# Kernel optimization log

Measured on AMD Instinct MI355X. Metric: run time of the kernel, lower is better.

Reference implementation:

```python
import jax, jax.numpy as jnp
import numpy as np

HIDDEN = 4096
N_HEADS = 32
N_KV_HEADS = 8
HEAD_DIM = 128
ROPE_THETA = 10000.0
LCK = 3          # number of suffix KV blocks
B = 2
S = 1024         # Q_LEN
VALID = 960      # valid_seq_len
NEG = -1e30


def rotate_half(x):
    h = x.shape[-1] // 2
    return jnp.concatenate([-x[..., h:], x[..., :h]], axis=-1)


def rope_cos_sin(seq_len, dim, theta, dtype):
    inv_freq = 1.0 / (theta ** (jnp.arange(0, dim, 2, dtype=jnp.float32) / dim))
    pos = jnp.arange(seq_len, dtype=jnp.float32)
    freqs = pos[:, None] * inv_freq[None, :]          # [S, dim/2]
    emb = jnp.concatenate([freqs, freqs], axis=-1)    # [S, dim]
    return jnp.cos(emb).astype(dtype), jnp.sin(emb).astype(dtype)


def setup_inputs() -> dict:
    key = jax.random.key(0)
    ks = jax.random.split(key, 8)
    w = 0.02
    return {
        "hidden_states": jax.random.normal(ks[0], (B, S, HIDDEN), jnp.float32),
        "k_suffix": jax.random.normal(ks[1], (B, N_KV_HEADS, LCK, S, HEAD_DIM), jnp.float32),
        "v_suffix": jax.random.normal(ks[2], (B, N_KV_HEADS, LCK, S, HEAD_DIM), jnp.float32),
        "Wq": jax.random.normal(ks[3], (HIDDEN, N_HEADS * HEAD_DIM), jnp.float32) * w,
        "Wk": jax.random.normal(ks[4], (HIDDEN, N_KV_HEADS * HEAD_DIM), jnp.float32) * w,
        "Wv": jax.random.normal(ks[5], (HIDDEN, N_KV_HEADS * HEAD_DIM), jnp.float32) * w,
        "Wo": jax.random.normal(ks[6], (N_HEADS * HEAD_DIM, HIDDEN), jnp.float32) * w,
        "valid_seq_len": VALID,
    }


def reference(hidden_states, k_suffix, v_suffix, Wq, Wk, Wv, Wo, valid_seq_len):
    b, s, _ = hidden_states.shape
    lck = k_suffix.shape[2]
    n_rep = N_HEADS // N_KV_HEADS
    scale = 1.0 / np.sqrt(HEAD_DIM)

    # projections: [B, H, S, D]
    q = (hidden_states @ Wq).reshape(b, s, N_HEADS, HEAD_DIM).transpose(0, 2, 1, 3)
    k0 = (hidden_states @ Wk).reshape(b, s, N_KV_HEADS, HEAD_DIM).transpose(0, 2, 1, 3)
    v0 = (hidden_states @ Wv).reshape(b, s, N_KV_HEADS, HEAD_DIM).transpose(0, 2, 1, 3)

    # RoPE on fresh q / k0
    cos, sin = rope_cos_sin(s, HEAD_DIM, ROPE_THETA, q.dtype)
    cos = cos[None, None]
    sin = sin[None, None]
    q = q * cos + rotate_half(q) * sin
    k0 = k0 * cos + rotate_half(k0) * sin

    # GQA expansion (repeat_kv)
    k0r = jnp.repeat(k0, n_rep, axis=1)                 # [B, H, S, D]
    v0r = jnp.repeat(v0, n_rep, axis=1)
    ks = jnp.repeat(k_suffix, n_rep, axis=1)            # [B, H, lck, S, D]
    vs = jnp.repeat(v_suffix, n_rep, axis=1)

    q_idx = jnp.arange(s)
    q_valid = q_idx < valid_seq_len                     # [S]

    # --- causal block (kv_idx < Q_LEN) ---
    sc_c = jnp.einsum('bhqd,bhkd->bhqk', q, k0r) * scale
    mask_c = (q_idx[:, None] >= q_idx[None, :]) & q_valid[None, :] & q_valid[:, None]
    sc_c = jnp.where(mask_c[None, None], sc_c, NEG)

    # --- suffix blocks: only diagonal kv_idx = q_idx + j*Q_LEN survives ---
    # score for suffix block j at query q is q . k_suffix[j, q]
    sc_s = jnp.einsum('bhqd,bhjqd->bhqj', q, ks) * scale    # [B, H, S, lck]
    # diag kv_mod == q_idx, so suffix valid iff q_idx < valid_seq_len
    sc_s = jnp.where(q_valid[None, None, :, None], sc_s, NEG)

    logits = jnp.concatenate([sc_c, sc_s], axis=-1)      # [B, H, S, S+lck]
    probs = jax.nn.softmax(logits, axis=-1)

    out = jnp.einsum('bhqk,bhkd->bhqd', probs[..., :s], v0r) + \
          jnp.einsum('bhqj,bhjqd->bhqd', probs[..., s:], vs)
    # fully-masked rows (q >= valid_seq_len) output zero like flash attention
    out = out * q_valid[None, None, :, None].astype(out.dtype)

    out = out.transpose(0, 2, 1, 3).reshape(b, s, N_HEADS * HEAD_DIM)
    return out @ Wo


if __name__ == "__main__":
    o = reference(**setup_inputs())
    print(o.shape, o.dtype)
```

## Files before the change

### kernel.cpp

```cpp
#include <hip/hip_runtime.h>

#define HIDDEN 4096
#define NH 32
#define NKV 8
#define HD 128
#define LCK 3
#define BB 2
#define SS 1024
#define MTOT (BB * SS)

typedef unsigned short u16;
typedef __attribute__((ext_vector_type(8))) short s16x8;
typedef __attribute__((ext_vector_type(4))) short s16x4;
typedef __attribute__((ext_vector_type(4))) float f32x4;

__device__ __forceinline__ u16 f2bf(float f) {
  unsigned u = __builtin_bit_cast(unsigned, f);
  u += 0x7fffu + ((u >> 16) & 1u);
  return (u16)(u >> 16);
}
__device__ __forceinline__ float bf2f(u16 h) {
  return __builtin_bit_cast(float, (unsigned)h << 16);
}
__device__ __forceinline__ void gld16(const void* g, void* l) {
  __builtin_amdgcn_global_load_lds((const __attribute__((address_space(1))) void*)g,
                                   (__attribute__((address_space(3))) void*)l, 16, 0, 0);
}

__global__ __launch_bounds__(256) void convert_h(const float* __restrict__ in,
                                                 u16* __restrict__ out, int n4) {
  int i = blockIdx.x * 256 + threadIdx.x;
  if (i >= n4) return;
  float4 v = ((const float4*)in)[i];
  uint2 o;
  o.x = (unsigned)f2bf(v.x) | ((unsigned)f2bf(v.y) << 16);
  o.y = (unsigned)f2bf(v.z) | ((unsigned)f2bf(v.w) << 16);
  ((uint2*)out)[i] = o;
}

__global__ __launch_bounds__(256) void transpose_w(const float* __restrict__ W,
                                                   u16* __restrict__ Wt, int K, int N) {
  __shared__ float tile[64][65];
  const int n0 = blockIdx.x * 64, k0 = blockIdx.y * 64;
  const int ty = threadIdx.x >> 6, tx = threadIdx.x & 63;
#pragma unroll
  for (int i = 0; i < 16; ++i) {
    int r = ty * 16 + i;
    tile[r][tx] = W[(size_t)(k0 + r) * N + n0 + tx];
  }
  __syncthreads();
#pragma unroll
  for (int i = 0; i < 16; ++i) {
    int r = ty * 16 + i;
    Wt[(size_t)(n0 + r) * K + k0 + tx] = f2bf(tile[tx][r]);
  }
}

template <bool BF16OUT>
__global__ __launch_bounds__(512, 2) void gemm_bt(
    const u16* __restrict__ A, const u16* __restrict__ Bt,
    void* C0v, void* C1v, void* C2v, int N, int K, int n1, int n2) {
  __shared__ __align__(16) char smem[131072];
  const int tid = threadIdx.x, lane = tid & 63, w = tid >> 6;
  const int wr = w >> 2, wc = w & 3;
  const int col16 = lane & 15, quad = lane >> 4;

  const int nbx = gridDim.x;
  const int nwg = nbx * gridDim.y;
  int fid = blockIdx.y * nbx + blockIdx.x;
  {
    const int q = nwg >> 3, r = nwg & 7;
    const int xcd = fid & 7, lid = fid >> 3;
    fid = (xcd < r ? xcd * (q + 1) : r * (q + 1) + (xcd - r) * q) + lid;
  }
  const int bm = (fid / nbx) << 8, bn = (fid % nbx) << 8;

  const int rowlane = lane >> 2;
  const int collane = ((lane & 3) * 8) ^ ((lane & 32) ? 16 : 0);
  const u16* aSrc = A + (size_t)(bm + ((w >> 1) << 4) + rowlane) * K + ((w & 1) << 5) + collane;
  const u16* bSrc = Bt + (size_t)(bn + ((w >> 1) << 4) + rowlane) * K + ((w & 1) << 5) + collane;
  const int laneoff = (lane & 15) * 64 + (((lane >> 4) << 4) ^ ((lane & 8) << 2));
  const int NT = K >> 6;

#define STG(opOfs, src, buf, h, tt)                                              \
  do {                                                                           \
    gld16((src) + (size_t)((h) * 128) * K + (size_t)(tt) * 64,                   \
          smem + (buf) * 65536 + (opOfs) +                                       \
              ((((h) * 8 + (w >> 1)) * 2 + (w & 1)) << 10));                     \
    gld16((src) + (size_t)((h) * 128 + 64) * K + (size_t)(tt) * 64,              \
          smem + (buf) * 65536 + (opOfs) +                                       \
              ((((h) * 8 + 4 + (w >> 1)) * 2 + (w & 1)) << 10));                 \
  } while (0)
#define BARX asm volatile("s_barrier" ::: "memory")
#define LGK0                                                                     \
  do {                                                                           \
    asm volatile("s_waitcnt lgkmcnt(0)" ::: "memory");                           \
    __builtin_amdgcn_sched_barrier(0);                                           \
  } while (0)

  f32x4 acc[8][4];
#pragma unroll
  for (int f = 0; f < 8; ++f)
#pragma unroll
    for (int g = 0; g < 4; ++g) acc[f][g] = (f32x4){0.f, 0.f, 0.f, 0.f};

  STG(32768, bSrc, 0, 0, 0);
  STG(32768, bSrc, 0, 1, 0);
  STG(0, aSrc, 0, 0, 0);
  STG(0, aSrc, 0, 1, 0);
  STG(32768, bSrc, 1, 0, 1);
  STG(32768, bSrc, 1, 1, 1);
  STG(0, aSrc, 1, 0, 1);
  asm volatile("s_waitcnt vmcnt(6)" ::: "memory");
  BARX;

  for (int kt = 0; kt < NT; ++kt) {
    const int buf = kt & 1;
    const char* Af = smem + buf * 65536 + wr * 16384 + laneoff;
    const char* Bf = smem + buf * 65536 + 32768 + wc * 8192 + laneoff;
    s16x8 b0[4], b1[4], a0[4], a1[4];
#pragma unroll
    for (int g = 0; g < 4; ++g) {
      b0[g] = *(const s16x8*)(Bf + (g * 2 + 0) * 1024);
      b1[g] = *(const s16x8*)(Bf + (g * 2 + 1) * 1024);
    }
#pragma unroll
    for (int f = 0; f < 4; ++f) a0[f] = *(const s16x8*)(Af + (f * 2 + 0) * 1024);
    if (kt + 1 < NT) STG(0, aSrc, (kt + 1) & 1, 1, kt + 1);
    BARX; LGK0;
    __builtin_amdgcn_s_setprio(1);
#pragma unroll
    for (int f = 0; f < 4; ++f)
#pragma unroll
      for (int g = 0; g < 4; ++g)
        acc[f][g] = __builtin_amdgcn_mfma_f32_16x16x32_bf16(a0[f], b0[g], acc[f][g], 0, 0, 0);
    __builtin_amdgcn_s_setprio(0);
    BARX;
#pragma unroll
    for (int f = 0; f < 4; ++f) a1[f] = *(const s16x8*)(Af + ((4 + f) * 2 + 0) * 1024);
#pragma unroll
    for (int f = 0; f < 4; ++f) a0[f] = *(const s16x8*)(Af + (f * 2 + 1) * 1024);
    if (kt + 2 < NT) STG(32768, bSrc, buf, 0, kt + 2);
    BARX; LGK0;
    __builtin_amdgcn_s_setprio(1);
#pragma unroll
    for (int f = 0; f < 4; ++f)
#pragma unroll
      for (int g = 0; g < 4; ++g)
        acc[4 + f][g] = __builtin_amdgcn_mfma_f32_16x16x32_bf16(a1[f], b0[g], acc[4 + f][g], 0, 0, 0);
    __builtin_amdgcn_s_setprio(0);
    BARX;
#pragma unroll
    for (int f = 0; f < 4; ++f) a1[f] = *(const s16x8*)(Af + ((4 + f) * 2 + 1) * 1024);
    if (kt + 2 < NT) STG(32768, bSrc, buf, 1, kt + 2);
    BARX; LGK0;
    __builtin_amdgcn_s_setprio(1);
#pragma unroll
    for (int f = 0; f < 4; ++f)
#pragma unroll
      for (int g = 0; g < 4; ++g)
        acc[f][g] = __builtin_amdgcn_mfma_f32_16x16x32_bf16(a0[f], b1[g], acc[f][g], 0, 0, 0);
    __builtin_amdgcn_s_setprio(0);
    BARX;
    if (kt + 2 < NT) STG(0, aSrc, buf, 0, kt + 2);
    BARX; LGK0;
    __builtin_amdgcn_s_setprio(1);
#pragma unroll
    for (int f = 0; f < 4; ++f)
#pragma unroll
      for (int g = 0; g < 4; ++g)
        acc[4 + f][g] = __builtin_amdgcn_mfma_f32_16x16x32_bf16(a1[f], b1[g], acc[4 + f][g], 0, 0, 0);
    __builtin_amdgcn_s_setprio(0);
    if (kt < NT - 2) asm volatile("s_waitcnt vmcnt(6)" ::: "memory");
    else if (kt == NT - 2) asm volatile("s_waitcnt vmcnt(0)" ::: "memory");
    BARX;
  }
#undef STG
#undef BARX
#undef LGK0

  float* Cf; u16* Ch; int ldc, nb;
  if (bn < n1)      { ldc = n1;      nb = bn;      Cf = (float*)C0v; Ch = (u16*)C0v; }
  else if (bn < n2) { ldc = n2 - n1; nb = bn - n1; Cf = (float*)C1v; Ch = (u16*)C1v; }
  else              { ldc = N - n2;  nb = bn - n2; Cf = (float*)C2v; Ch = (u16*)C2v; }
#pragma unroll
  for (int f = 0; f < 8; ++f)
#pragma unroll
    for (int g = 0; g < 4; ++g)
#pragma unroll
      for (int r = 0; r < 4; ++r) {
        size_t off = (size_t)(bm + wr * 128 + f * 16 + quad * 4 + r) * ldc +
                     nb + wc * 64 + g * 16 + col16;
        if (BF16OUT) Ch[off] = f2bf(acc[f][g][r]);
        else         Cf[off] = acc[f][g][r];
      }
}

__global__ __launch_bounds__(256) void rope_convert(const u16* __restrict__ Qin,
                                                    const u16* __restrict__ Kin,
                                                    u16* __restrict__ Qout,
                                                    u16* __restrict__ Kout) {
  const int per_row = (NH + NKV) * 64;
  int idx = blockIdx.x * 256 + threadIdx.x;
  if (idx >= MTOT * per_row) return;
  int row = idx / per_row;
  int rem = idx - row * per_row;
  int hh = rem >> 6, i = rem & 63;
  int s = row & (SS - 1), b = row >> 10;

  float invf = __expf((float)i * (-9.210340371976184f / 64.0f));
  float ang = (float)s * invf;
  float cv = cosf(ang), sv = sinf(ang);

  if (hh < NH) {
    const u16* src = Qin + (size_t)row * (NH * HD) + hh * HD;
    u16* dst = Qout + (((size_t)(b * NH + hh)) * SS + s) * HD;
    float x0 = bf2f(src[i]), x1 = bf2f(src[i + 64]);
    dst[i] = f2bf(x0 * cv - x1 * sv);
    dst[i + 64] = f2bf(x1 * cv + x0 * sv);
  } else {
    int kh = hh - NH;
    const u16* src = Kin + (size_t)row * (NKV * HD) + kh * HD;
    u16* dst = Kout + (((size_t)(b * NKV + kh)) * SS + s) * HD;
    float x0 = bf2f(src[i]), x1 = bf2f(src[i + 64]);
    dst[i] = f2bf(x0 * cv - x1 * sv);
    dst[i + 64] = f2bf(x1 * cv + x0 * sv);
  }
}

__global__ __launch_bounds__(256) void transpose_v(const u16* __restrict__ V0,
                                                   u16* __restrict__ Vt) {
  __shared__ u16 tile[64][65];
  const int s0 = blockIdx.x * 64, d0 = blockIdx.y * 64;
  const int bk = blockIdx.z;
  const int b = bk >> 3, kvh = bk & 7;
  const int ty = threadIdx.x >> 6, tx = threadIdx.x & 63;
#pragma unroll
  for (int i = 0; i < 16; ++i) {
    int r = ty * 16 + i;
    tile[r][tx] = V0[((size_t)(b * SS + s0 + r)) * (NKV * HD) + kvh * HD + d0 + tx];
  }
  __syncthreads();
#pragma unroll
  for (int i = 0; i < 16; ++i) {
    int r = ty * 16 + i;
    Vt[((size_t)bk * HD + d0 + r) * SS + s0 + tx] = tile[tx][r];
  }
}

__global__ __launch_bounds__(256) void attn_mfma(
    const u16* __restrict__ Qbf, const u16* __restrict__ Kbf, const u16* __restrict__ Vt,
    const float* __restrict__ ksuf, const float* __restrict__ vsuf,
    u16* __restrict__ AObf, const int* __restrict__ validp) {
  __shared__ __align__(16) char Ksm[2][16384];
  __shared__ __align__(16) char Vsm[2][16384];

  const int bid = (int)blockIdx.x;
  const int qt = 63 - (bid >> 4);
  const int kvh = bid & 7, b = (bid >> 3) & 1;
  const int q0 = qt * 16;
  const int lane = threadIdx.x & 63, w = threadIdx.x >> 6;
  const int col = lane & 15, quad = lane >> 4;
  const int h = (kvh << 2) + w;
  const int valid = *validp;
  const int q = q0 + col;

  size_t orow = ((size_t)(b * SS + q)) * (NH * HD) + h * HD;
  if (q0 >= valid) {
    ushort4 z = {0, 0, 0, 0};
#pragma unroll
    for (int nt = 0; nt < 8; ++nt)
      *(ushort4*)(AObf + orow + 16 * nt + quad * 4) = z;
    return;
  }

  const float scale = 0.08838834764831845f;
  const u16* qptr = Qbf + (((size_t)(b * NH + h)) * SS + q) * HD;
  s16x8 qf[4];
#pragma unroll
  for (int ds = 0; ds < 4; ++ds) qf[ds] = *(const s16x8*)(qptr + ds * 32 + quad * 8);

  const u16* kbase = Kbf + ((size_t)(b * NKV + kvh)) * SS * HD;
  const u16* vbase = Vt + ((size_t)(b * NKV + kvh)) * HD * SS;

  int ksrcoff[4], vsrcoff[4];
  {
    const int kq = (w * 4 + quad) & 7;
    const int dq = (lane >> 3) & 7;
#pragma unroll
    for (int j = 0; j < 4; ++j) {
      int kl = j * 16 + w * 4 + quad;
      ksrcoff[j] = kl * HD + (((col * 16) ^ (kq << 4)) >> 1);
      int dl = j * 32 + w * 8 + (lane >> 3);
      vsrcoff[j] = dl * SS + ((((lane & 7) * 16) ^ (dq << 4)) >> 1);
    }
  }

#define STAGE(bufi, k0v)                                                        \
  do {                                                                          \
    const u16* kp_ = kbase + (size_t)(k0v)*HD;                                  \
    const u16* vp_ = vbase + (k0v);                                             \
    _Pragma("unroll") for (int j = 0; j < 4; ++j)                               \
        gld16(kp_ + ksrcoff[j], Ksm[bufi] + j * 4096 + w * 1024);               \
    _Pragma("unroll") for (int j = 0; j < 4; ++j)                               \
        gld16(vp_ + vsrcoff[j], Vsm[bufi] + j * 4096 + w * 1024);               \
  } while (0)

  float m_ = -1e30f, l_ = 0.f;
  f32x4 O_[8];
#pragma unroll
  for (int nt = 0; nt < 8; ++nt) O_[nt] = (f32x4){0.f, 0.f, 0.f, 0.f};

  const int ntiles = (q0 + 16 + 63) >> 6;
  const int kswz = (col & 7) << 4;

  STAGE(0, 0);
  __syncthreads();

  for (int ti = 0; ti < ntiles; ++ti) {
    const int k0 = ti * 64;
    if (ti + 1 < ntiles) STAGE((ti + 1) & 1, k0 + 64);
    const char* Kb = Ksm[ti & 1];
    const char* Vb = Vsm[ti & 1];

    f32x4 S[4];
#pragma unroll
    for (int ks = 0; ks < 4; ++ks) {
      f32x4 s = (f32x4){0.f, 0.f, 0.f, 0.f};
#pragma unroll
      for (int ds = 0; ds < 4; ++ds) {
        s16x8 kf = *(const s16x8*)(Kb + ks * 4096 + col * 256 +
                                   ((ds * 64 + quad * 16) ^ kswz));
        s = __builtin_amdgcn_mfma_f32_16x16x32_bf16(kf, qf[ds], s, 0, 0, 0);
      }
      S[ks] = s;
    }
    float sc[16];
    float tm = -1e30f;
#pragma unroll
    for (int ks = 0; ks < 4; ++ks)
#pragma unroll
      for (int r = 0; r < 4; ++r) {
        int kg = k0 + ks * 16 + quad * 4 + r;
        float v = (kg > q) ? -1e30f : S[ks][r] * scale;
        sc[ks * 4 + r] = v;
        tm = fmaxf(tm, v);
      }
    tm = fmaxf(tm, __shfl_xor(tm, 16));
    tm = fmaxf(tm, __shfl_xor(tm, 32));
    float mn = fmaxf(m_, tm);
    float a = __expf(m_ - mn);
    float pv[16];
    float rs = 0.f;
#pragma unroll
    for (int i = 0; i < 16; ++i) {
      pv[i] = __expf(sc[i] - mn);
      rs += pv[i];
    }
    rs += __shfl_xor(rs, 16);
    rs += __shfl_xor(rs, 32);
    l_ = l_ * a + rs;
    m_ = mn;
#pragma unroll
    for (int nt = 0; nt < 8; ++nt)
#pragma unroll
      for (int r = 0; r < 4; ++r) O_[nt][r] *= a;

#pragma unroll
    for (int ks = 0; ks < 4; ++ks) {
      s16x8 pb;
      pb[0] = (short)f2bf(pv[ks * 4 + 0]);
      pb[1] = (short)f2bf(pv[ks * 4 + 1]);
      pb[2] = (short)f2bf(pv[ks * 4 + 2]);
      pb[3] = (short)f2bf(pv[ks * 4 + 3]);
      pb[4] = 0; pb[5] = 0; pb[6] = 0; pb[7] = 0;
#pragma unroll
      for (int nt = 0; nt < 8; ++nt) {
        s16x4 vv = *(const s16x4*)(Vb + nt * 2048 + col * 128 +
                                   ((ks * 32 + quad * 8) ^ kswz));
        s16x8 av;
        av[0] = vv[0]; av[1] = vv[1]; av[2] = vv[2]; av[3] = vv[3];
        av[4] = 0; av[5] = 0; av[6] = 0; av[7] = 0;
        O_[nt] = __builtin_amdgcn_mfma_f32_16x16x32_bf16(av, pb, O_[nt], 0, 0, 0);
      }
    }
    __syncthreads();
  }
#undef STAGE

  float sp[3];
#pragma unroll
  for (int j = 0; j < 3; ++j) {
    const float* kr = ksuf + ((((size_t)(b * NKV + kvh) * LCK + j)) * SS + q) * HD + quad * 8;
    float p = 0.f;
#pragma unroll
    for (int ds = 0; ds < 4; ++ds)
#pragma unroll
      for (int e = 0; e < 8; ++e) p += bf2f((u16)qf[ds][e]) * kr[ds * 32 + e];
    p += __shfl_xor(p, 16);
    p += __shfl_xor(p, 32);
    sp[j] = p * scale;
  }
  {
    float ms = fmaxf(fmaxf(sp[0], sp[1]), sp[2]);
    float mn = fmaxf(m_, ms);
    float a = __expf(m_ - mn);
    float e0 = __expf(sp[0] - mn);
    float e1 = __expf(sp[1] - mn);
    float e2 = __expf(sp[2] - mn);
    l_ = l_ * a + e0 + e1 + e2;
    const float* v0r = vsuf + ((((size_t)(b * NKV + kvh) * LCK + 0)) * SS + q) * HD + quad * 4;
    const float* v1r = v0r + (size_t)SS * HD;
    const float* v2r = v1r + (size_t)SS * HD;
#pragma unroll
    for (int nt = 0; nt < 8; ++nt) {
      float4 x0 = *(const float4*)(v0r + 16 * nt);
      float4 x1 = *(const float4*)(v1r + 16 * nt);
      float4 x2 = *(const float4*)(v2r + 16 * nt);
      O_[nt][0] = O_[nt][0] * a + e0 * x0.x + e1 * x1.x + e2 * x2.x;
      O_[nt][1] = O_[nt][1] * a + e0 * x0.y + e1 * x1.y + e2 * x2.y;
      O_[nt][2] = O_[nt][2] * a + e0 * x0.z + e1 * x1.z + e2 * x2.z;
      O_[nt][3] = O_[nt][3] * a + e0 * x0.w + e1 * x1.w + e2 * x2.w;
    }
  }

  if (q >= valid) {
    ushort4 z = {0, 0, 0, 0};
#pragma unroll
    for (int nt = 0; nt < 8; ++nt)
      *(ushort4*)(AObf + orow + 16 * nt + quad * 4) = z;
  } else {
    float inv = 1.f / l_;
#pragma unroll
    for (int nt = 0; nt < 8; ++nt) {
      ushort4 o;
      o.x = f2bf(O_[nt][0] * inv);
      o.y = f2bf(O_[nt][1] * inv);
      o.z = f2bf(O_[nt][2] * inv);
      o.w = f2bf(O_[nt][3] * inv);
      *(ushort4*)(AObf + orow + 16 * nt + quad * 4) = o;
    }
  }
}

extern "C" void kernel_launch(void* const* d_in, const int* in_sizes, int n_in,
                              void* d_out, int out_size, void* d_ws, size_t ws_size,
                              hipStream_t stream) {
  const float* hidden = (const float*)d_in[0];
  const float* ksuf = (const float*)d_in[1];
  const float* vsuf = (const float*)d_in[2];
  const float* Wq = (const float*)d_in[3];
  const float* Wk = (const float*)d_in[4];
  const float* Wv = (const float*)d_in[5];
  const float* Wo = (const float*)d_in[6];
  const int* validp = (const int*)d_in[7];
  float* out = (float*)d_out;

  char* W = (char*)d_ws;
  u16* Hbf  = (u16*)(W + 0);
  u16* WqT  = (u16*)(W + ((size_t)16 << 20));
  u16* WkT  = (u16*)(W + ((size_t)48 << 20));
  u16* WvT  = (u16*)(W + ((size_t)56 << 20));
  u16* Qbf0 = (u16*)(W + ((size_t)64 << 20));
  u16* K0bf = (u16*)(W + ((size_t)80 << 20));
  u16* V0bf = (u16*)(W + ((size_t)84 << 20));
  u16* Kbf  = (u16*)(W + ((size_t)88 << 20));
  u16* Vt   = (u16*)(W + ((size_t)92 << 20));
  u16* Qbf  = (u16*)(W + 0);
  u16* WoT  = (u16*)(W + ((size_t)16 << 20));
  u16* AObf = (u16*)(W + ((size_t)64 << 20));

  convert_h<<<(MTOT * HIDDEN / 4 + 255) / 256, 256, 0, stream>>>(hidden, Hbf, MTOT * HIDDEN / 4);
  transpose_w<<<dim3(64, 64), 256, 0, stream>>>(Wq, WqT, HIDDEN, NH * HD);
  transpose_w<<<dim3(16, 64), 256, 0, stream>>>(Wk, WkT, HIDDEN, NKV * HD);
  transpose_w<<<dim3(16, 64), 256, 0, stream>>>(Wv, WvT, HIDDEN, NKV * HD);
  gemm_bt<true><<<dim3(24, 8), 512, 0, stream>>>(
      Hbf, WqT, Qbf0, K0bf, V0bf, 6144, HIDDEN, 4096, 5120);
  transpose_w<<<dim3(64, 64), 256, 0, stream>>>(Wo, WoT, NH * HD, HIDDEN);
  rope_convert<<<(MTOT * (NH + NKV) * 64 + 255) / 256, 256, 0, stream>>>(Qbf0, K0bf, Qbf, Kbf);
  transpose_v<<<dim3(16, 2, BB * NKV), 256, 0, stream>>>(V0bf, Vt);
  attn_mfma<<<dim3(1024), 256, 0, stream>>>(Qbf, Kbf, Vt, ksuf, vsuf, AObf, validp);
  gemm_bt<false><<<dim3(16, 8), 512, 0, stream>>>(
      AObf, WoT, out, out, out, HIDDEN, NH * HD, 4096, 4096);
}
```

Baseline: 538.5 us.

## Split-K the output projection, reschedule A-tile prefetch, vectorize RoPE kernel

```diff
diff --git a/kernel.cpp b/kernel.cpp
--- a/kernel.cpp
+++ b/kernel.cpp
@@ -38,6 +38,16 @@
   ((uint2*)out)[i] = o;
 }
 
+__global__ __launch_bounds__(256) void add2(float* __restrict__ out,
+                                            const float* __restrict__ P, int n4) {
+  int i = blockIdx.x * 256 + threadIdx.x;
+  if (i >= n4) return;
+  float4 a = ((const float4*)out)[i];
+  float4 b = ((const float4*)P)[i];
+  a.x += b.x; a.y += b.y; a.z += b.z; a.w += b.w;
+  ((float4*)out)[i] = a;
+}
+
 __global__ __launch_bounds__(256) void transpose_w(const float* __restrict__ W,
                                                    u16* __restrict__ Wt, int K, int N) {
   __shared__ float tile[64][65];
@@ -56,7 +66,7 @@
   }
 }
 
-template <bool BF16OUT>
+template <bool BF16OUT, bool SPLITK>
 __global__ __launch_bounds__(512, 2) void gemm_bt(
     const u16* __restrict__ A, const u16* __restrict__ Bt,
     void* C0v, void* C1v, void* C2v, int N, int K, int n1, int n2) {
@@ -64,6 +74,8 @@
   const int tid = threadIdx.x, lane = tid & 63, w = tid >> 6;
   const int wr = w >> 2, wc = w & 3;
   const int col16 = lane & 15, quad = lane >> 4;
+  const int kz = SPLITK ? (int)blockIdx.z : 0;
+  const int Keff = SPLITK ? (K >> 1) : K;
 
   const int nbx = gridDim.x;
   const int nwg = nbx * gridDim.y;
@@ -77,10 +89,12 @@
 
   const int rowlane = lane >> 2;
   const int collane = ((lane & 3) * 8) ^ ((lane & 32) ? 16 : 0);
-  const u16* aSrc = A + (size_t)(bm + ((w >> 1) << 4) + rowlane) * K + ((w & 1) << 5) + collane;
-  const u16* bSrc = Bt + (size_t)(bn + ((w >> 1) << 4) + rowlane) * K + ((w & 1) << 5) + collane;
+  const u16* aSrc = A + (size_t)(bm + ((w >> 1) << 4) + rowlane) * K + ((w & 1) << 5) + collane +
+                    (size_t)kz * Keff;
+  const u16* bSrc = Bt + (size_t)(bn + ((w >> 1) << 4) + rowlane) * K + ((w & 1) << 5) + collane +
+                    (size_t)kz * Keff;
   const int laneoff = (lane & 15) * 64 + (((lane >> 4) << 4) ^ ((lane & 8) << 2));
-  const int NT = K >> 6;
+  const int NT = Keff >> 6;
 
 #define STG(opOfs, src, buf, h, tt)                                              \
   do {                                                                           \
@@ -111,7 +125,8 @@
   STG(32768, bSrc, 1, 0, 1);
   STG(32768, bSrc, 1, 1, 1);
   STG(0, aSrc, 1, 0, 1);
-  asm volatile("s_waitcnt vmcnt(6)" ::: "memory");
+  STG(0, aSrc, 1, 1, 1);
+  asm volatile("s_waitcnt vmcnt(8)" ::: "memory");
   BARX;
 
   for (int kt = 0; kt < NT; ++kt) {
@@ -126,7 +141,6 @@
     }
 #pragma unroll
     for (int f = 0; f < 4; ++f) a0[f] = *(const s16x8*)(Af + (f * 2 + 0) * 1024);
-    if (kt + 1 < NT) STG(0, aSrc, (kt + 1) & 1, 1, kt + 1);
     BARX; LGK0;
     __builtin_amdgcn_s_setprio(1);
 #pragma unroll
@@ -162,7 +176,10 @@
         acc[f][g] = __builtin_amdgcn_mfma_f32_16x16x32_bf16(a0[f], b1[g], acc[f][g], 0, 0, 0);
     __builtin_amdgcn_s_setprio(0);
     BARX;
-    if (kt + 2 < NT) STG(0, aSrc, buf, 0, kt + 2);
+    if (kt + 2 < NT) {
+      STG(0, aSrc, buf, 0, kt + 2);
+      STG(0, aSrc, buf, 1, kt + 2);
+    }
     BARX; LGK0;
     __builtin_amdgcn_s_setprio(1);
 #pragma unroll
@@ -171,7 +188,7 @@
       for (int g = 0; g < 4; ++g)
         acc[4 + f][g] = __builtin_amdgcn_mfma_f32_16x16x32_bf16(a1[f], b1[g], acc[4 + f][g], 0, 0, 0);
     __builtin_amdgcn_s_setprio(0);
-    if (kt < NT - 2) asm volatile("s_waitcnt vmcnt(6)" ::: "memory");
+    if (kt < NT - 2) asm volatile("s_waitcnt vmcnt(8)" ::: "memory");
     else if (kt == NT - 2) asm volatile("s_waitcnt vmcnt(0)" ::: "memory");
     BARX;
   }
@@ -180,9 +197,11 @@
 #undef LGK0
 
   float* Cf; u16* Ch; int ldc, nb;
-  if (bn < n1)      { ldc = n1;      nb = bn;      Cf = (float*)C0v; Ch = (u16*)C0v; }
-  else if (bn < n2) { ldc = n2 - n1; nb = bn - n1; Cf = (float*)C1v; Ch = (u16*)C1v; }
-  else              { ldc = N - n2;  nb = bn - n2; Cf = (float*)C2v; Ch = (u16*)C2v; }
+  if (SPLITK) {
+    Cf = (float*)(kz ? C1v : C0v); Ch = (u16*)Cf; ldc = N; nb = bn;
+  } else if (bn < n1) { ldc = n1;      nb = bn;      Cf = (float*)C0v; Ch = (u16*)C0v; }
+  else if (bn < n2)   { ldc = n2 - n1; nb = bn - n1; Cf = (float*)C1v; Ch = (u16*)C1v; }
+  else                { ldc = N - n2;  nb = bn - n2; Cf = (float*)C2v; Ch = (u16*)C2v; }
 #pragma unroll
   for (int f = 0; f < 8; ++f)
 #pragma unroll
@@ -200,32 +219,43 @@
                                                     const u16* __restrict__ Kin,
                                                     u16* __restrict__ Qout,
                                                     u16* __restrict__ Kout) {
-  const int per_row = (NH + NKV) * 64;
+  const int per_row = (NH + NKV) * 16;
   int idx = blockIdx.x * 256 + threadIdx.x;
   if (idx >= MTOT * per_row) return;
   int row = idx / per_row;
   int rem = idx - row * per_row;
-  int hh = rem >> 6, i = rem & 63;
+  int hh = rem >> 4, t4 = rem & 15;
   int s = row & (SS - 1), b = row >> 10;
-
-  float invf = __expf((float)i * (-9.210340371976184f / 64.0f));
-  float ang = (float)s * invf;
-  float cv = cosf(ang), sv = sinf(ang);
-
+  int i0 = t4 * 4;
+
+  const u16* src; u16* dst;
   if (hh < NH) {
-    const u16* src = Qin + (size_t)row * (NH * HD) + hh * HD;
-    u16* dst = Qout + (((size_t)(b * NH + hh)) * SS + s) * HD;
-    float x0 = bf2f(src[i]), x1 = bf2f(src[i + 64]);
-    dst[i] = f2bf(x0 * cv - x1 * sv);
-    dst[i + 64] = f2bf(x1 * cv + x0 * sv);
+    src = Qin + (size_t)row * (NH * HD) + hh * HD;
+    dst = Qout + (((size_t)(b * NH + hh)) * SS + s) * HD;
   } else {
     int kh = hh - NH;
-    const u16* src = Kin + (size_t)row * (NKV * HD) + kh * HD;
-    u16* dst = Kout + (((size_t)(b * NKV + kh)) * SS + s) * HD;
-    float x0 = bf2f(src[i]), x1 = bf2f(src[i + 64]);
-    dst[i] = f2bf(x0 * cv - x1 * sv);
-    dst[i + 64] = f2bf(x1 * cv + x0 * sv);
-  }
+    src = Kin + (size_t)row * (NKV * HD) + kh * HD;
+    dst = Kout + (((size_t)(b * NKV + kh)) * SS + s) * HD;
+  }
+  ushort4 x0 = *(const ushort4*)(src + i0);
+  ushort4 x1 = *(const ushort4*)(src + i0 + 64);
+  const u16* xa0 = (const u16*)&x0;
+  const u16* xa1 = (const u16*)&x1;
+  ushort4 o0, o1;
+  u16* oa0 = (u16*)&o0;
+  u16* oa1 = (u16*)&o1;
+#pragma unroll
+  for (int j = 0; j < 4; ++j) {
+    float invf = __expf((float)(i0 + j) * (-9.210340371976184f / 64.0f));
+    float ang = (float)s * invf;
+    float sv, cv;
+    __sincosf(ang, &sv, &cv);
+    float a0 = bf2f(xa0[j]), a1 = bf2f(xa1[j]);
+    oa0[j] = f2bf(a0 * cv - a1 * sv);
+    oa1[j] = f2bf(a1 * cv + a0 * sv);
+  }
+  *(ushort4*)(dst + i0) = o0;
+  *(ushort4*)(dst + i0 + 64) = o1;
 }
 
 __global__ __launch_bounds__(256) void transpose_v(const u16* __restrict__ V0,
@@ -468,18 +498,20 @@
   u16* Vt   = (u16*)(W + ((size_t)92 << 20));
   u16* Qbf  = (u16*)(W + 0);
   u16* WoT  = (u16*)(W + ((size_t)16 << 20));
-  u16* AObf = (u16*)(W + ((size_t)64 << 20));
+  u16* AObf = (u16*)(W + ((size_t)48 << 20));
+  float* P1f = (float*)(W + ((size_t)64 << 20));
 
   convert_h<<<(MTOT * HIDDEN / 4 + 255) / 256, 256, 0, stream>>>(hidden, Hbf, MTOT * HIDDEN / 4);
   transpose_w<<<dim3(64, 64), 256, 0, stream>>>(Wq, WqT, HIDDEN, NH * HD);
   transpose_w<<<dim3(16, 64), 256, 0, stream>>>(Wk, WkT, HIDDEN, NKV * HD);
   transpose_w<<<dim3(16, 64), 256, 0, stream>>>(Wv, WvT, HIDDEN, NKV * HD);
-  gemm_bt<true><<<dim3(24, 8), 512, 0, stream>>>(
+  gemm_bt<true, false><<<dim3(24, 8), 512, 0, stream>>>(
       Hbf, WqT, Qbf0, K0bf, V0bf, 6144, HIDDEN, 4096, 5120);
   transpose_w<<<dim3(64, 64), 256, 0, stream>>>(Wo, WoT, NH * HD, HIDDEN);
-  rope_convert<<<(MTOT * (NH + NKV) * 64 + 255) / 256, 256, 0, stream>>>(Qbf0, K0bf, Qbf, Kbf);
+  rope_convert<<<(MTOT * (NH + NKV) * 16 + 255) / 256, 256, 0, stream>>>(Qbf0, K0bf, Qbf, Kbf);
   transpose_v<<<dim3(16, 2, BB * NKV), 256, 0, stream>>>(V0bf, Vt);
   attn_mfma<<<dim3(1024), 256, 0, stream>>>(Qbf, Kbf, Vt, ksuf, vsuf, AObf, validp);
-  gemm_bt<false><<<dim3(16, 8), 512, 0, stream>>>(
-      AObf, WoT, out, out, out, HIDDEN, NH * HD, 4096, 4096);
-}
+  gemm_bt<false, true><<<dim3(16, 8, 2), 512, 0, stream>>>(
+      AObf, WoT, out, P1f, nullptr, HIDDEN, NH * HD, HIDDEN, HIDDEN);
+  add2<<<(MTOT * HIDDEN / 4 + 255) / 256, 256, 0, stream>>>(out, P1f, MTOT * HIDDEN / 4);
+}
```

Measured after the change: 512.4 us. 4.9% less time.
